# Optimization experiments

Hardware: AMD Instinct MI355X
Metric: run time of the kernel (lower is better)

The kernel has to match this reference:

```python
import jax, jax.numpy as jnp
import numpy as np

B, S, H, E, D, K = 2, 2048, 2048, 8, 2048, 2


def setup_inputs() -> dict:
    key = jax.random.key(0)
    ks = jax.random.split(key, 4)
    # lecun_normal-style scaling: std = 1/sqrt(fan_in)
    return {
        "x": jax.random.normal(ks[0], (B, S, H), jnp.float32),
        "router_w": jax.random.normal(ks[1], (H, E), jnp.float32) / np.sqrt(H).astype(np.float32),
        "router_b": jnp.zeros((E,), jnp.float32),
        "expert_w": jax.random.normal(ks[2], (E, H, D), jnp.float32) / np.sqrt(H).astype(np.float32),
        "expert_b": jnp.zeros((E, D), jnp.float32),
        "out_w": jax.random.normal(ks[3], (D, D), jnp.float32) / np.sqrt(D).astype(np.float32),
        "out_b": jnp.zeros((D,), jnp.float32),
    }


def reference(x, router_w, router_b, expert_w, expert_b, out_w, out_b):
    num_experts = expert_w.shape[0]
    # Router: logits -> softmax -> top-2 -> renormalize
    router_logits = jnp.einsum("bsh,he->bse", x, router_w) + router_b
    router_probs = jax.nn.softmax(router_logits, axis=-1)
    top_k_probs, top_k_indices = jax.lax.top_k(router_probs, K)  # [B,S,K]
    top_k_probs = top_k_probs / jnp.sum(top_k_probs, axis=-1, keepdims=True)
    # Per-expert gate weight: sum of top-k probs routed to that expert. [B,S,E]
    onehot = jax.nn.one_hot(top_k_indices, num_experts, dtype=x.dtype)  # [B,S,K,E]
    gates = jnp.einsum("bsk,bske->bse", top_k_probs, onehot)
    # Dense per-expert GEMM + gelu (mask-and-multiply MoE; gate==0 kills unrouted tokens)
    expert_out = jax.nn.gelu(jnp.einsum("bsh,ehd->ebsd", x, expert_w) + expert_b[:, None, None, :])
    combined = jnp.einsum("bse,ebsd->bsd", gates, expert_out)
    # Output projection
    return jnp.einsum("bsd,df->bsf", combined, out_w) + out_b
```

## Files before the change

### kernel.cpp

```cpp
#include <hip/hip_runtime.h>
#include <stdint.h>

#define H_DIM 2048
#define E_NUM 8
#define D_DIM 2048
#define NTOK 4096
#define BM 128
#define BN 128
#define BK 32

typedef __bf16 bf16x8 __attribute__((ext_vector_type(8)));
typedef float f32x4 __attribute__((ext_vector_type(4)));

__device__ __forceinline__ unsigned short f2bf(float f) {
    union { float f; uint32_t u; } c; c.f = f;
    uint32_t r = (c.u + 0x7FFFu + ((c.u >> 16) & 1u)) >> 16;
    return (unsigned short)r;
}
__device__ __forceinline__ float bf2f(unsigned short h) {
    union { float f; uint32_t u; } c; c.u = ((uint32_t)h) << 16;
    return c.f;
}

__device__ __forceinline__ void gl_lds16(const unsigned short* g, unsigned short* l) {
    __builtin_amdgcn_global_load_lds(
        (const __attribute__((address_space(1))) unsigned int*)g,
        (__attribute__((address_space(3))) unsigned int*)l, 16, 0, 0);
}

__global__ __launch_bounds__(256) void router_cvt_kernel(
    const float* __restrict__ x, const float* __restrict__ rw,
    const float* __restrict__ rb, int* __restrict__ counts,
    uint32_t* __restrict__ tok, float* __restrict__ gate,
    unsigned short* __restrict__ xb) {
    int t = (blockIdx.x * 256 + threadIdx.x) >> 6;
    int lane = threadIdx.x & 63;
    const float* xr = x + (size_t)t * H_DIM;
    unsigned short* xo = xb + (size_t)t * H_DIM;
    float p[E_NUM];
#pragma unroll
    for (int e = 0; e < E_NUM; e++) p[e] = 0.f;
#pragma unroll
    for (int pass = 0; pass < H_DIM / 256; pass++) {
        int h = pass * 256 + lane * 4;
        float4 v = *(const float4*)(xr + h);
        ushort4 o;
        o.x = f2bf(v.x); o.y = f2bf(v.y); o.z = f2bf(v.z); o.w = f2bf(v.w);
        *(ushort4*)(xo + h) = o;
        const float* r0 = rw + (size_t)h * E_NUM;
#pragma unroll
        for (int e = 0; e < E_NUM; e++)
            p[e] += v.x * r0[e] + v.y * r0[e + 8] + v.z * r0[e + 16] + v.w * r0[e + 24];
    }
#pragma unroll
    for (int e = 0; e < E_NUM; e++) {
#pragma unroll
        for (int off = 1; off < 64; off <<= 1) p[e] += __shfl_xor(p[e], off, 64);
    }
    if (lane == 0) {
        float l[E_NUM];
#pragma unroll
        for (int e = 0; e < E_NUM; e++) l[e] = p[e] + rb[e];
        int e0 = 0;
#pragma unroll
        for (int e = 1; e < E_NUM; e++) if (l[e] > l[e0]) e0 = e;
        int e1 = (e0 == 0) ? 1 : 0;
#pragma unroll
        for (int e = 0; e < E_NUM; e++) if (e != e0 && l[e] > l[e1]) e1 = e;
        float g0 = 1.f / (1.f + __expf(l[e1] - l[e0]));
        float g1 = 1.f - g0;
        int p0 = atomicAdd(&counts[e0], 1);
        tok[e0 * NTOK + p0] = (uint32_t)t;
        gate[e0 * NTOK + p0] = g0;
        int p1 = atomicAdd(&counts[e1], 1);
        tok[e1 * NTOK + p1] = (uint32_t)t | (1u << 16);
        gate[e1 * NTOK + p1] = g1;
    }
}

__global__ __launch_bounds__(256) void transpose_cvt_kernel(
    const float* __restrict__ ew, const float* __restrict__ ow,
    unsigned short* __restrict__ ewT) {
    __shared__ unsigned short t[64][136];
    int z = blockIdx.z;
    const float* s = (z < 8) ? (ew + (size_t)z * H_DIM * D_DIM) : ow;
    unsigned short* d = ewT + (size_t)z * H_DIM * D_DIM;
    int n0 = blockIdx.x * 64, k0 = blockIdx.y * 128;
    int tid = threadIdx.x;
    int rr = tid >> 4;
    int c4 = (tid & 15) * 4;
#pragma unroll
    for (int p = 0; p < 8; p++) {
        int k = p * 16 + rr;
        float4 v = *(const float4*)(s + (size_t)(k0 + k) * D_DIM + n0 + c4);
        t[c4 + 0][k] = f2bf(v.x);
        t[c4 + 1][k] = f2bf(v.y);
        t[c4 + 2][k] = f2bf(v.z);
        t[c4 + 3][k] = f2bf(v.w);
    }
    __syncthreads();
    int kc = (tid & 15) * 8;
#pragma unroll
    for (int p = 0; p < 4; p++) {
        int n = p * 16 + rr;
        uint4 v = *(const uint4*)&t[n][kc];
        *(uint4*)(d + (size_t)(n0 + n) * H_DIM + k0 + kc) = v;
    }
}

__global__ __launch_bounds__(256) void expert_gemm_kernel(
    const unsigned short* __restrict__ xb,
    const unsigned short* __restrict__ ewT,
    const float* __restrict__ eb,
    const int* __restrict__ counts,
    const uint32_t* __restrict__ tok,
    const float* __restrict__ gate,
    unsigned short* __restrict__ Y)
{
    int e = blockIdx.z;
    int cnt = counts[e];
    int m0 = blockIdx.y * BM;
    if (m0 >= cnt) return;
    int n0 = blockIdx.x * BN;

    __shared__ unsigned short As[BM][BK];
    __shared__ unsigned short Bs[BN][BK];
    __shared__ uint32_t tok_s[BM];
    __shared__ float gate_s[BM];

    int tid = threadIdx.x;
    if (tid < BM) {
        int idx = m0 + tid;
        uint32_t tk = 0; float g = 0.f;
        if (idx < cnt) { tk = tok[e * NTOK + idx]; g = gate[e * NTOK + idx]; }
        tok_s[tid] = tk; gate_s[tid] = g;
    }
    __syncthreads();

    int lane = tid & 63;
    int wave = tid >> 6;
    int sr = lane >> 2;
    int sc = ((lane & 3) ^ ((lane >> 3) & 3)) * 8;
    int r0 = wave * 32 + sr;
    int r1 = wave * 32 + 16 + sr;
    const unsigned short* agp0 = xb + (size_t)(tok_s[r0] & 0xFFFFu) * H_DIM + sc;
    const unsigned short* agp1 = xb + (size_t)(tok_s[r1] & 0xFFFFu) * H_DIM + sc;
    const unsigned short* bbase = ewT + (size_t)e * D_DIM * H_DIM;
    const unsigned short* bgp0 = bbase + (size_t)(n0 + r0) * H_DIM + sc;
    const unsigned short* bgp1 = bbase + (size_t)(n0 + r1) * H_DIM + sc;
    unsigned short* la0 = &As[wave * 32][0];
    unsigned short* la1 = &As[wave * 32 + 16][0];
    unsigned short* lb0 = &Bs[wave * 32][0];
    unsigned short* lb1 = &Bs[wave * 32 + 16][0];

    int wm = (wave >> 1) * 64;
    int wn = (wave & 1) * 64;
    int row16 = lane & 15;
    int quad = lane >> 4;
    int slot = (quad ^ ((row16 >> 1) & 3)) * 16;
    int aoffA[4], aoffB[4];
#pragma unroll
    for (int i = 0; i < 4; i++) {
        aoffA[i] = (wm + i * 16 + row16) * (BK * 2) + slot;
        aoffB[i] = (wn + i * 16 + row16) * (BK * 2) + slot;
    }
    const char* pA = (const char*)&As[0][0];
    const char* pB = (const char*)&Bs[0][0];

    f32x4 acc[4][4];
#pragma unroll
    for (int i = 0; i < 4; i++)
#pragma unroll
        for (int j = 0; j < 4; j++) acc[i][j] = (f32x4)(0.f);

    for (int kk = 0; kk < H_DIM; kk += BK) {
        __syncthreads();
        gl_lds16(agp0 + kk, la0);
        gl_lds16(agp1 + kk, la1);
        gl_lds16(bgp0 + kk, lb0);
        gl_lds16(bgp1 + kk, lb1);
        __syncthreads();
        bf16x8 af[4], bff[4];
#pragma unroll
        for (int i = 0; i < 4; i++) {
            af[i] = *(const bf16x8*)(pA + aoffA[i]);
            bff[i] = *(const bf16x8*)(pB + aoffB[i]);
        }
#pragma unroll
        for (int i = 0; i < 4; i++)
#pragma unroll
            for (int j = 0; j < 4; j++)
                acc[i][j] = __builtin_amdgcn_mfma_f32_16x16x32_bf16(
                    af[i], bff[j], acc[i][j], 0, 0, 0);
    }

#pragma unroll
    for (int i = 0; i < 4; i++) {
        int rbase = wm + i * 16 + quad * 4;
#pragma unroll
        for (int j = 0; j < 4; j++) {
            int n = n0 + wn + j * 16 + row16;
            float bias = eb[e * D_DIM + n];
#pragma unroll
            for (int r = 0; r < 4; r++) {
                int lrow = rbase + r;
                if (m0 + lrow < cnt) {
                    uint32_t tk = tok_s[lrow];
                    float g = gate_s[lrow];
                    float v = acc[i][j][r] + bias;
                    float q = 0.7978845608028654f * (v + 0.044715f * v * v * v);
                    float gl = v / (1.f + __expf(-2.f * q));
                    int token = tk & 0xFFFF;
                    int slot2 = (tk >> 16) & 1;
                    Y[((size_t)token * 2 + slot2) * D_DIM + n] = f2bf(g * gl);
                }
            }
        }
    }
}

__global__ __launch_bounds__(256) void combine_kernel(
    const unsigned short* __restrict__ Y, unsigned short* __restrict__ comb) {
    int i = blockIdx.x * 256 + threadIdx.x;
    int t = i >> 8;
    int dc = (i & 255) * 8;
    uint4 u0 = *(const uint4*)(Y + (size_t)t * 2 * D_DIM + dc);
    uint4 u1 = *(const uint4*)(Y + ((size_t)t * 2 + 1) * D_DIM + dc);
    uint4 o;
    uint32_t* po = (uint32_t*)&o;
    const uint32_t* p0 = (const uint32_t*)&u0;
    const uint32_t* p1 = (const uint32_t*)&u1;
#pragma unroll
    for (int k = 0; k < 4; k++) {
        uint32_t a = p0[k], b = p1[k];
        float s0 = bf2f((unsigned short)(a & 0xFFFF)) + bf2f((unsigned short)(b & 0xFFFF));
        float s1 = bf2f((unsigned short)(a >> 16)) + bf2f((unsigned short)(b >> 16));
        po[k] = (uint32_t)f2bf(s0) | ((uint32_t)f2bf(s1) << 16);
    }
    *(uint4*)(comb + (size_t)t * D_DIM + dc) = o;
}

__global__ __launch_bounds__(256) void out_gemm_kernel(
    const unsigned short* __restrict__ comb,
    const unsigned short* __restrict__ owT,
    const float* __restrict__ ob,
    float* __restrict__ out) {
    int m0 = blockIdx.y * BM, n0 = blockIdx.x * BN;
    __shared__ unsigned short As[BM][BK];
    __shared__ unsigned short Bs[BN][BK];
    int tid = threadIdx.x;
    int lane = tid & 63;
    int wave = tid >> 6;
    int sr = lane >> 2;
    int sc = ((lane & 3) ^ ((lane >> 3) & 3)) * 8;
    int r0 = wave * 32 + sr;
    int r1 = wave * 32 + 16 + sr;
    const unsigned short* agp0 = comb + (size_t)(m0 + r0) * D_DIM + sc;
    const unsigned short* agp1 = comb + (size_t)(m0 + r1) * D_DIM + sc;
    const unsigned short* bgp0 = owT + (size_t)(n0 + r0) * D_DIM + sc;
    const unsigned short* bgp1 = owT + (size_t)(n0 + r1) * D_DIM + sc;
    unsigned short* la0 = &As[wave * 32][0];
    unsigned short* la1 = &As[wave * 32 + 16][0];
    unsigned short* lb0 = &Bs[wave * 32][0];
    unsigned short* lb1 = &Bs[wave * 32 + 16][0];

    int wm = (wave >> 1) * 64;
    int wn = (wave & 1) * 64;
    int row16 = lane & 15;
    int quad = lane >> 4;
    int slot = (quad ^ ((row16 >> 1) & 3)) * 16;
    int aoffA[4], aoffB[4];
#pragma unroll
    for (int i = 0; i < 4; i++) {
        aoffA[i] = (wm + i * 16 + row16) * (BK * 2) + slot;
        aoffB[i] = (wn + i * 16 + row16) * (BK * 2) + slot;
    }
    const char* pA = (const char*)&As[0][0];
    const char* pB = (const char*)&Bs[0][0];

    f32x4 acc[4][4];
#pragma unroll
    for (int i = 0; i < 4; i++)
#pragma unroll
        for (int j = 0; j < 4; j++) acc[i][j] = (f32x4)(0.f);

    for (int kk = 0; kk < D_DIM; kk += BK) {
        __syncthreads();
        gl_lds16(agp0 + kk, la0);
        gl_lds16(agp1 + kk, la1);
        gl_lds16(bgp0 + kk, lb0);
        gl_lds16(bgp1 + kk, lb1);
        __syncthreads();
        bf16x8 af[4], bff[4];
#pragma unroll
        for (int i = 0; i < 4; i++) {
            af[i] = *(const bf16x8*)(pA + aoffA[i]);
            bff[i] = *(const bf16x8*)(pB + aoffB[i]);
        }
#pragma unroll
        for (int i = 0; i < 4; i++)
#pragma unroll
            for (int j = 0; j < 4; j++)
                acc[i][j] = __builtin_amdgcn_mfma_f32_16x16x32_bf16(
                    af[i], bff[j], acc[i][j], 0, 0, 0);
    }

#pragma unroll
    for (int i = 0; i < 4; i++) {
        int rbase = m0 + wm + i * 16 + quad * 4;
#pragma unroll
        for (int j = 0; j < 4; j++) {
            int n = n0 + wn + j * 16 + row16;
            float bias = ob[n];
#pragma unroll
            for (int r = 0; r < 4; r++) {
                out[(size_t)(rbase + r) * D_DIM + n] = acc[i][j][r] + bias;
            }
        }
    }
}

extern "C" void kernel_launch(void* const* d_in, const int* in_sizes, int n_in,
                              void* d_out, int out_size, void* d_ws, size_t ws_size,
                              hipStream_t stream) {
    const float* x        = (const float*)d_in[0];
    const float* router_w = (const float*)d_in[1];
    const float* router_b = (const float*)d_in[2];
    const float* expert_w = (const float*)d_in[3];
    const float* expert_b = (const float*)d_in[4];
    const float* out_w    = (const float*)d_in[5];
    const float* out_b    = (const float*)d_in[6];
    float* out = (float*)d_out;

    char* w = (char*)d_ws;
    int* counts = (int*)w;
    uint32_t* tok = (uint32_t*)(w + 1024);
    float* gate = (float*)(w + 1024 + E_NUM * NTOK * 4);
    size_t off = 1024 + (size_t)2 * E_NUM * NTOK * 4;
    unsigned short* xb = (unsigned short*)(w + off);
    off += (size_t)NTOK * H_DIM * 2;
    unsigned short* ewT = (unsigned short*)(w + off);
    off += (size_t)E_NUM * H_DIM * D_DIM * 2;
    unsigned short* owT = (unsigned short*)(w + off);
    off += (size_t)D_DIM * D_DIM * 2;
    unsigned short* Y = (unsigned short*)(w + off);
    off += (size_t)NTOK * 2 * D_DIM * 2;
    unsigned short* comb = (unsigned short*)(w + off);

    hipMemsetAsync(d_ws, 0, 1024, stream);
    router_cvt_kernel<<<NTOK / 4, 256, 0, stream>>>(x, router_w, router_b,
                                                    counts, tok, gate, xb);
    transpose_cvt_kernel<<<dim3(32, 16, 9), 256, 0, stream>>>(expert_w, out_w, ewT);
    expert_gemm_kernel<<<dim3(16, 32, 8), 256, 0, stream>>>(
        xb, ewT, expert_b, counts, tok, gate, Y);
    combine_kernel<<<NTOK * D_DIM / 8 / 256, 256, 0, stream>>>(Y, comb);
    out_gemm_kernel<<<dim3(16, 32), 256, 0, stream>>>(comb, owT, out_b, out);
}
```

Measured before the change: 528.1 us.

## Replace both GEMMs with a double-buffered 8-wave 128x256 pipelined kernel

Replaces the two 128x128, BK=32 single-buffered GEMM kernels with one templated kernel. It uses 512 threads, 128x256 tiles, BK=64, double-buffered LDS with global-to-LDS prefetch two tiles ahead, XOR swizzling, and an interleaved schedule of LDS reads and MFMA quarters using manual waitcnt, barriers and setprio. The goal is to hide global memory latency behind MFMA work and raise data reuse per block. In exchange it needs about 96KB of LDS per block and a fragile hand-tuned schedule with manual vmcnt accounting.

```diff
diff --git a/kernel.cpp b/kernel.cpp
--- a/kernel.cpp
+++ b/kernel.cpp
@@ -5,9 +5,6 @@
 #define E_NUM 8
 #define D_DIM 2048
 #define NTOK 4096
-#define BM 128
-#define BN 128
-#define BK 32
 
 typedef __bf16 bf16x8 __attribute__((ext_vector_type(8)));
 typedef float f32x4 __attribute__((ext_vector_type(4)));
@@ -108,115 +105,189 @@
     }
 }
 
-__global__ __launch_bounds__(256) void expert_gemm_kernel(
-    const unsigned short* __restrict__ xb,
-    const unsigned short* __restrict__ ewT,
-    const float* __restrict__ eb,
+
+#define GBAR() __builtin_amdgcn_s_barrier()
+#define LGKM0() do { asm volatile("s_waitcnt lgkmcnt(0)" ::: "memory"); \
+                     __builtin_amdgcn_sched_barrier(0); } while (0)
+#define VMW(N) asm volatile("s_waitcnt vmcnt(" #N ")" ::: "memory")
+
+template <int MOE>
+__global__ __launch_bounds__(512, 2) void gemm8p_kernel(
+    const unsigned short* __restrict__ Amat,
+    const unsigned short* __restrict__ Bmat,
+    const float* __restrict__ bias,
     const int* __restrict__ counts,
     const uint32_t* __restrict__ tok,
     const float* __restrict__ gate,
-    unsigned short* __restrict__ Y)
-{
-    int e = blockIdx.z;
-    int cnt = counts[e];
-    int m0 = blockIdx.y * BM;
-    if (m0 >= cnt) return;
-    int n0 = blockIdx.x * BN;
-
-    __shared__ unsigned short As[BM][BK];
-    __shared__ unsigned short Bs[BN][BK];
-    __shared__ uint32_t tok_s[BM];
-    __shared__ float gate_s[BM];
-
-    int tid = threadIdx.x;
-    if (tid < BM) {
-        int idx = m0 + tid;
-        uint32_t tk = 0; float g = 0.f;
-        if (idx < cnt) { tk = tok[e * NTOK + idx]; g = gate[e * NTOK + idx]; }
-        tok_s[tid] = tk; gate_s[tid] = g;
-    }
-    __syncthreads();
-
-    int lane = tid & 63;
-    int wave = tid >> 6;
-    int sr = lane >> 2;
-    int sc = ((lane & 3) ^ ((lane >> 3) & 3)) * 8;
-    int r0 = wave * 32 + sr;
-    int r1 = wave * 32 + 16 + sr;
-    const unsigned short* agp0 = xb + (size_t)(tok_s[r0] & 0xFFFFu) * H_DIM + sc;
-    const unsigned short* agp1 = xb + (size_t)(tok_s[r1] & 0xFFFFu) * H_DIM + sc;
-    const unsigned short* bbase = ewT + (size_t)e * D_DIM * H_DIM;
-    const unsigned short* bgp0 = bbase + (size_t)(n0 + r0) * H_DIM + sc;
-    const unsigned short* bgp1 = bbase + (size_t)(n0 + r1) * H_DIM + sc;
-    unsigned short* la0 = &As[wave * 32][0];
-    unsigned short* la1 = &As[wave * 32 + 16][0];
-    unsigned short* lb0 = &Bs[wave * 32][0];
-    unsigned short* lb1 = &Bs[wave * 32 + 16][0];
-
-    int wm = (wave >> 1) * 64;
-    int wn = (wave & 1) * 64;
-    int row16 = lane & 15;
-    int quad = lane >> 4;
-    int slot = (quad ^ ((row16 >> 1) & 3)) * 16;
-    int aoffA[4], aoffB[4];
-#pragma unroll
-    for (int i = 0; i < 4; i++) {
-        aoffA[i] = (wm + i * 16 + row16) * (BK * 2) + slot;
-        aoffB[i] = (wn + i * 16 + row16) * (BK * 2) + slot;
-    }
-    const char* pA = (const char*)&As[0][0];
-    const char* pB = (const char*)&Bs[0][0];
-
+    unsigned short* __restrict__ Ybf,
+    float* __restrict__ outF) {
+    constexpr int KD = 2048;
+    constexpr int NT = KD / 64;
+
+    __shared__ unsigned short sA[2][128 * 64];
+    __shared__ unsigned short sB[2][256 * 64];
+    __shared__ uint32_t tok_s[128];
+    __shared__ float gate_s[128];
+
+    const int e = MOE ? blockIdx.z : 0;
+    const int cnt = MOE ? counts[e] : NTOK;
+    const int m0 = blockIdx.y * 128;
+    if (MOE && m0 >= cnt) return;
+    const int n0 = blockIdx.x * 256;
+    const int tid = threadIdx.x;
+
+    if (MOE) {
+        if (tid < 128) {
+            int idx = m0 + tid;
+            uint32_t tk = 0; float g = 0.f;
+            if (idx < cnt) { tk = tok[e * NTOK + idx]; g = gate[e * NTOK + idx]; }
+            tok_s[tid] = tk; gate_s[tid] = g;
+        }
+        __syncthreads();
+    }
+
+    const unsigned short* Bp = Bmat + (size_t)e * D_DIM * KD;
+
+    const int rr = tid >> 3;
+    const int swz = ((tid & 7) ^ (rr & 7)) * 8;
+    uint32_t aOff[2], bOff[4];
+#pragma unroll
+    for (int l = 0; l < 2; l++) {
+        int r = l * 64 + rr;
+        uint32_t arow = MOE ? (tok_s[r] & 0xFFFFu) : (uint32_t)(m0 + r);
+        aOff[l] = arow * (uint32_t)KD + swz;
+    }
+#pragma unroll
+    for (int h = 0; h < 2; h++)
+#pragma unroll
+        for (int l = 0; l < 2; l++) {
+            int r = h * 128 + l * 64 + rr;
+            bOff[h * 2 + l] = (uint32_t)(n0 + r) * (uint32_t)KD + swz;
+        }
+
+    const int lane = tid & 63;
+    const int wave = tid >> 6;
+    const int wm = wave >> 2;
+    const int wn = wave & 3;
+    const int row16 = lane & 15;
+    const int quad = lane >> 4;
+    const int baseA = (wm * 64 + row16) * 64;
+    const int baseB = (wn * 64 + row16) * 64;
+    const int xo0 = ((quad) ^ (lane & 7)) * 8;
+    const int xo1 = ((4 + quad) ^ (lane & 7)) * 8;
+    const int wbase = wave * 512;
+
+#define STG_A(BUF, T) do { \
+        gl_lds16(Amat + aOff[0] + (T) * 64, &sA[BUF][wbase]); \
+        gl_lds16(Amat + aOff[1] + (T) * 64, &sA[BUF][4096 + wbase]); } while (0)
+#define STG_B(BUF, HH, T) do { \
+        gl_lds16(Bp + bOff[(HH) * 2 + 0] + (T) * 64, &sB[BUF][(HH) * 8192 + wbase]); \
+        gl_lds16(Bp + bOff[(HH) * 2 + 1] + (T) * 64, &sB[BUF][(HH) * 8192 + 4096 + wbase]); } while (0)
+
+    bf16x8 aLo[2][2], aHi[2][2], bLo[2][2], bHi[2][2];
     f32x4 acc[4][4];
 #pragma unroll
     for (int i = 0; i < 4; i++)
 #pragma unroll
         for (int j = 0; j < 4; j++) acc[i][j] = (f32x4)(0.f);
 
-    for (int kk = 0; kk < H_DIM; kk += BK) {
-        __syncthreads();
-        gl_lds16(agp0 + kk, la0);
-        gl_lds16(agp1 + kk, la1);
-        gl_lds16(bgp0 + kk, lb0);
-        gl_lds16(bgp1 + kk, lb1);
-        __syncthreads();
-        bf16x8 af[4], bff[4];
-#pragma unroll
-        for (int i = 0; i < 4; i++) {
-            af[i] = *(const bf16x8*)(pA + aoffA[i]);
-            bff[i] = *(const bf16x8*)(pB + aoffB[i]);
-        }
-#pragma unroll
-        for (int i = 0; i < 4; i++)
-#pragma unroll
-            for (int j = 0; j < 4; j++)
-                acc[i][j] = __builtin_amdgcn_mfma_f32_16x16x32_bf16(
-                    af[i], bff[j], acc[i][j], 0, 0, 0);
-    }
-
-#pragma unroll
-    for (int i = 0; i < 4; i++) {
-        int rbase = wm + i * 16 + quad * 4;
-#pragma unroll
-        for (int j = 0; j < 4; j++) {
-            int n = n0 + wn + j * 16 + row16;
-            float bias = eb[e * D_DIM + n];
-#pragma unroll
-            for (int r = 0; r < 4; r++) {
-                int lrow = rbase + r;
-                if (m0 + lrow < cnt) {
-                    uint32_t tk = tok_s[lrow];
-                    float g = gate_s[lrow];
-                    float v = acc[i][j][r] + bias;
-                    float q = 0.7978845608028654f * (v + 0.044715f * v * v * v);
-                    float gl = v / (1.f + __expf(-2.f * q));
-                    int token = tk & 0xFFFF;
-                    int slot2 = (tk >> 16) & 1;
-                    Y[((size_t)token * 2 + slot2) * D_DIM + n] = f2bf(g * gl);
+#define LOADA(DST, FB, BUF) do { _Pragma("unroll") \
+        for (int f_ = 0; f_ < 2; f_++) { \
+            DST[f_][0] = *(const bf16x8*)&sA[BUF][baseA + ((FB) + f_) * 1024 + xo0]; \
+            DST[f_][1] = *(const bf16x8*)&sA[BUF][baseA + ((FB) + f_) * 1024 + xo1]; } } while (0)
+#define LOADB(DST, FB, BUF) do { _Pragma("unroll") \
+        for (int c_ = 0; c_ < 2; c_++) { \
+            DST[c_][0] = *(const bf16x8*)&sB[BUF][baseB + ((FB) + c_) * 1024 + xo0]; \
+            DST[c_][1] = *(const bf16x8*)&sB[BUF][baseB + ((FB) + c_) * 1024 + xo1]; } } while (0)
+#define MFMAQ(AF, BF, FR, FC) do { _Pragma("unroll") \
+        for (int s_ = 0; s_ < 2; s_++) { _Pragma("unroll") \
+            for (int f_ = 0; f_ < 2; f_++) { _Pragma("unroll") \
+                for (int c_ = 0; c_ < 2; c_++) \
+                    acc[(FR) + f_][(FC) + c_] = __builtin_amdgcn_mfma_f32_16x16x32_bf16( \
+                        AF[f_][s_], BF[c_][s_], acc[(FR) + f_][(FC) + c_], 0, 0, 0); } } } while (0)
+
+#define TILE(BC, BN_, T, S1, S3, S4, VMLINE) do { \
+         \
+        LOADA(aLo, 0, BC); LOADB(bLo, 0, BC); \
+        if (S1) STG_B(BN_, 1, (T) + 1); \
+        GBAR(); LGKM0(); \
+        __builtin_amdgcn_s_setprio(1); MFMAQ(aLo, bLo, 0, 0); __builtin_amdgcn_s_setprio(0); \
+        GBAR(); \
+         \
+        LOADB(bHi, 2, BC); \
+        GBAR(); LGKM0(); \
+        __builtin_amdgcn_s_setprio(1); MFMAQ(aLo, bHi, 0, 2); __builtin_amdgcn_s_setprio(0); \
+        GBAR(); \
+         \
+        LOADA(aHi, 2, BC); \
+        if (S3) STG_B(BC, 0, (T) + 2); \
+        GBAR(); LGKM0(); \
+        __builtin_amdgcn_s_setprio(1); MFMAQ(aHi, bLo, 2, 0); __builtin_amdgcn_s_setprio(0); \
+        GBAR(); \
+         \
+        if (S4) STG_A(BC, (T) + 2); \
+        VMLINE; \
+        GBAR(); \
+        __builtin_amdgcn_s_setprio(1); MFMAQ(aHi, bHi, 2, 2); __builtin_amdgcn_s_setprio(0); \
+        GBAR(); } while (0)
+
+    STG_B(0, 0, 0); STG_B(0, 1, 0); STG_A(0, 0);
+    STG_B(1, 0, 1); STG_A(1, 1);
+    VMW(4);
+    GBAR();
+
+    int t0 = 0;
+#pragma unroll 1
+    for (int tp = 0; tp < NT / 2 - 1; ++tp, t0 += 2) {
+        TILE(0, 1, t0, 1, 1, 1, VMW(4));
+        TILE(1, 0, t0 + 1, 1, 1, 1, VMW(4));
+    }
+    TILE(0, 1, NT - 2, 1, 0, 0, VMW(0));
+    TILE(1, 0, NT - 1, 0, 0, 0, (void)0);
+
+    if (MOE) {
+#pragma unroll
+        for (int f = 0; f < 4; f++) {
+            const int rb = wm * 64 + f * 16 + quad * 4;
+#pragma unroll
+            for (int c = 0; c < 4; c++) {
+                const int n = n0 + wn * 64 + c * 16 + row16;
+                const float bv = bias[e * D_DIM + n];
+#pragma unroll
+                for (int r = 0; r < 4; r++) {
+                    const int lrow = rb + r;
+                    if (m0 + lrow < cnt) {
+                        const uint32_t tk = tok_s[lrow];
+                        const float g = gate_s[lrow];
+                        float v = acc[f][c][r] + bv;
+                        float q = 0.7978845608028654f * (v + 0.044715f * v * v * v);
+                        float gl = v / (1.f + __expf(-2.f * q));
+                        Ybf[((size_t)(tk & 0xFFFFu) * 2 + ((tk >> 16) & 1)) * D_DIM + n] =
+                            f2bf(g * gl);
+                    }
                 }
             }
         }
-    }
+    } else {
+#pragma unroll
+        for (int f = 0; f < 4; f++) {
+            const int rb = m0 + wm * 64 + f * 16 + quad * 4;
+#pragma unroll
+            for (int c = 0; c < 4; c++) {
+                const int n = n0 + wn * 64 + c * 16 + row16;
+                const float bv = bias[n];
+#pragma unroll
+                for (int r = 0; r < 4; r++)
+                    outF[(size_t)(rb + r) * D_DIM + n] = acc[f][c][r] + bv;
+            }
+        }
+    }
+#undef STG_A
+#undef STG_B
+#undef LOADA
+#undef LOADB
+#undef MFMAQ
+#undef TILE
 }
 
 __global__ __launch_bounds__(256) void combine_kernel(
@@ -238,86 +309,6 @@
         po[k] = (uint32_t)f2bf(s0) | ((uint32_t)f2bf(s1) << 16);
     }
     *(uint4*)(comb + (size_t)t * D_DIM + dc) = o;
-}
-
-__global__ __launch_bounds__(256) void out_gemm_kernel(
-    const unsigned short* __restrict__ comb,
-    const unsigned short* __restrict__ owT,
-    const float* __restrict__ ob,
-    float* __restrict__ out) {
-    int m0 = blockIdx.y * BM, n0 = blockIdx.x * BN;
-    __shared__ unsigned short As[BM][BK];
-    __shared__ unsigned short Bs[BN][BK];
-    int tid = threadIdx.x;
-    int lane = tid & 63;
-    int wave = tid >> 6;
-    int sr = lane >> 2;
-    int sc = ((lane & 3) ^ ((lane >> 3) & 3)) * 8;
-    int r0 = wave * 32 + sr;
-    int r1 = wave * 32 + 16 + sr;
-    const unsigned short* agp0 = comb + (size_t)(m0 + r0) * D_DIM + sc;
-    const unsigned short* agp1 = comb + (size_t)(m0 + r1) * D_DIM + sc;
-    const unsigned short* bgp0 = owT + (size_t)(n0 + r0) * D_DIM + sc;
-    const unsigned short* bgp1 = owT + (size_t)(n0 + r1) * D_DIM + sc;
-    unsigned short* la0 = &As[wave * 32][0];
-    unsigned short* la1 = &As[wave * 32 + 16][0];
-    unsigned short* lb0 = &Bs[wave * 32][0];
-    unsigned short* lb1 = &Bs[wave * 32 + 16][0];
-
-    int wm = (wave >> 1) * 64;
-    int wn = (wave & 1) * 64;
-    int row16 = lane & 15;
-    int quad = lane >> 4;
-    int slot = (quad ^ ((row16 >> 1) & 3)) * 16;
-    int aoffA[4], aoffB[4];
-#pragma unroll
-    for (int i = 0; i < 4; i++) {
-        aoffA[i] = (wm + i * 16 + row16) * (BK * 2) + slot;
-        aoffB[i] = (wn + i * 16 + row16) * (BK * 2) + slot;
-    }
-    const char* pA = (const char*)&As[0][0];
-    const char* pB = (const char*)&Bs[0][0];
-
-    f32x4 acc[4][4];
-#pragma unroll
-    for (int i = 0; i < 4; i++)
-#pragma unroll
-        for (int j = 0; j < 4; j++) acc[i][j] = (f32x4)(0.f);
-
-    for (int kk = 0; kk < D_DIM; kk += BK) {
-        __syncthreads();
-        gl_lds16(agp0 + kk, la0);
-        gl_lds16(agp1 + kk, la1);
-        gl_lds16(bgp0 + kk, lb0);
-        gl_lds16(bgp1 + kk, lb1);
-        __syncthreads();
-        bf16x8 af[4], bff[4];
-#pragma unroll
-        for (int i = 0; i < 4; i++) {
-            af[i] = *(const bf16x8*)(pA + aoffA[i]);
-            bff[i] = *(const bf16x8*)(pB + aoffB[i]);
-        }
-#pragma unroll
-        for (int i = 0; i < 4; i++)
-#pragma unroll
-            for (int j = 0; j < 4; j++)
-                acc[i][j] = __builtin_amdgcn_mfma_f32_16x16x32_bf16(
-                    af[i], bff[j], acc[i][j], 0, 0, 0);
-    }
-
-#pragma unroll
-    for (int i = 0; i < 4; i++) {
-        int rbase = m0 + wm + i * 16 + quad * 4;
-#pragma unroll
-        for (int j = 0; j < 4; j++) {
-            int n = n0 + wn + j * 16 + row16;
-            float bias = ob[n];
-#pragma unroll
-            for (int r = 0; r < 4; r++) {
-                out[(size_t)(rbase + r) * D_DIM + n] = acc[i][j][r] + bias;
-            }
-        }
-    }
 }
 
 extern "C" void kernel_launch(void* const* d_in, const int* in_sizes, int n_in,
@@ -351,8 +342,9 @@
     router_cvt_kernel<<<NTOK / 4, 256, 0, stream>>>(x, router_w, router_b,
                                                     counts, tok, gate, xb);
     transpose_cvt_kernel<<<dim3(32, 16, 9), 256, 0, stream>>>(expert_w, out_w, ewT);
-    expert_gemm_kernel<<<dim3(16, 32, 8), 256, 0, stream>>>(
-        xb, ewT, expert_b, counts, tok, gate, Y);
+    gemm8p_kernel<1><<<dim3(8, 32, 8), 512, 0, stream>>>(
+        xb, ewT, expert_b, counts, tok, gate, Y, nullptr);
     combine_kernel<<<NTOK * D_DIM / 8 / 256, 256, 0, stream>>>(Y, comb);
-    out_gemm_kernel<<<dim3(16, 32), 256, 0, stream>>>(comb, owT, out_b, out);
-}
+    gemm8p_kernel<0><<<dim3(8, 32, 1), 512, 0, stream>>>(
+        comb, owT, out_b, nullptr, nullptr, nullptr, nullptr, out);
+}
```

After: 542.6 us. +2.7%, slower.
